# Kernel optimization log

Measured on AMD Instinct MI355X. Metric: run time of the kernel, lower is better.

Reference implementation:

```python
import jax, jax.numpy as jnp
import numpy as np

B, T, C, H = 4, 2048, 768, 12
D = C // H  # head_dim = 64
ROPE_BASE = 10000.0


def _make_rope_cache(seq_len, n_elem, base=ROPE_BASE):
    theta = 1.0 / base ** (jnp.arange(0, n_elem, 2, dtype=jnp.float32) / n_elem)  # [D/2]
    idx_theta = jnp.arange(seq_len, dtype=jnp.float32)[:, None] * theta[None, :]  # [T, D/2]
    return jnp.stack([jnp.cos(idx_theta), jnp.sin(idx_theta)], axis=-1)  # [T, D/2, 2]


def setup_inputs() -> dict:
    key = jax.random.key(0)
    k1, k2, k3 = jax.random.split(key, 3)
    x = jax.random.normal(k1, (B, T, C), dtype=jnp.float32)
    rope_cache = _make_rope_cache(T, D)
    w_qkv = jax.random.normal(k2, (3 * C, C), dtype=jnp.float32) * (1.0 / np.sqrt(C))
    w_o = jax.random.normal(k3, (C, C), dtype=jnp.float32) * (1.0 / np.sqrt(C))
    return {"x": x, "rope_cache": rope_cache, "w_qkv": w_qkv, "w_o": w_o}


def _apply_rope(t, cos, sin):
    # t: [B,T,H,D]; cos/sin: [T,D/2] broadcast to [1,T,1,D/2]
    tp = t.reshape(t.shape[:-1] + (D // 2, 2))
    t0, t1 = tp[..., 0], tp[..., 1]
    c = cos[None, :, None, :]
    s = sin[None, :, None, :]
    rot = jnp.stack([t0 * c - t1 * s, t0 * s + t1 * c], axis=-1)
    return rot.reshape(t.shape)


def reference(x, rope_cache, w_qkv, w_o):
    b, t, c = x.shape
    qkv = (x @ w_qkv.T).reshape(b, t, 3, H, D)
    q, k, v = qkv[:, :, 0], qkv[:, :, 1], qkv[:, :, 2]  # [B,T,H,D]
    cos = rope_cache[:t, :, 0]
    sin = rope_cache[:t, :, 1]
    q = _apply_rope(q, cos, sin)
    k = _apply_rope(k, cos, sin)
    scale = 1.0 / np.sqrt(D)
    att = jnp.einsum('bqhd,bkhd->bhqk', q, k) * scale  # [B,H,T,T]
    causal = jnp.tril(jnp.ones((t, t), dtype=bool))
    att = jnp.where(causal[None, None], att, jnp.finfo(att.dtype).min)
    att = jax.nn.softmax(att, axis=-1)
    y = jnp.einsum('bhqk,bkhd->bqhd', att, v).reshape(b, t, c)
    return y @ w_o.T
```

## Files before the change

kernel.cpp:

```cpp
#include <hip/hip_runtime.h>

#define B_  4
#define T_  2048
#define C_  768
#define H_  12
#define D_  64

typedef unsigned short u16;
typedef unsigned int   u32;
typedef __bf16 bf16;
typedef __bf16 bf16x4 __attribute__((ext_vector_type(4)));
typedef __bf16 bf16x8 __attribute__((ext_vector_type(8)));
typedef float  f32x4  __attribute__((ext_vector_type(4)));
typedef float  f32x16 __attribute__((ext_vector_type(16)));
typedef u32    u32x4  __attribute__((ext_vector_type(4)));
typedef __attribute__((address_space(1))) void* gas_t;
typedef __attribute__((address_space(3))) void* las_t;

static __device__ __forceinline__ u16 f2bf(float f) {
  u32 u = __builtin_bit_cast(u32, f);
  u += 0x7FFFu + ((u >> 16) & 1u);
  return (u16)(u >> 16);
}

static __device__ __forceinline__ u32 cvtpk(float a, float b) {
  u32 r;
  asm("v_cvt_pk_bf16_f32 %0, %1, %2" : "=v"(r) : "v"(a), "v"(b));
  return r;
}
static __device__ __forceinline__ void plswap(u32& a, u32& b) {
  asm volatile("v_permlane32_swap_b32 %0, %1" : "+v"(a), "+v"(b));
}

__global__ __launch_bounds__(256) void k_cvt3(const float* __restrict__ a0,
                                              const float* __restrict__ a1,
                                              const float* __restrict__ a2,
                                              u16* __restrict__ o0,
                                              u16* __restrict__ o1,
                                              u16* __restrict__ o2) {
  const int bid = blockIdx.x;
  const int tid = threadIdx.x;
  if (bid < 6144) {
    const int i = bid * 256 + tid;
    const float4 v = ((const float4*)a0)[i];
    ushort4 o;
    o.x = f2bf(v.x); o.y = f2bf(v.y); o.z = f2bf(v.z); o.w = f2bf(v.w);
    ((ushort4*)o0)[i] = o;
  } else if (bid < 7872) {
    const int i = (bid - 6144) * 256 + tid;
    const int n = i / 192;
    const int c4 = i - n * 192;
    int n2 = n;
    if (n < 1536) {
      const int d = n & 63;
      const int c = (((d & 1) | ((d >> 5) << 1)) << 4) | ((d >> 1) & 15);
      n2 = (n & ~63) | c;
    }
    const float4 v = ((const float4*)a1)[i];
    ushort4 o;
    o.x = f2bf(v.x); o.y = f2bf(v.y); o.z = f2bf(v.z); o.w = f2bf(v.w);
    ((ushort4*)o1)[n2 * 192 + c4] = o;
  } else {
    const int i = (bid - 7872) * 256 + tid;
    const float4 v = ((const float4*)a2)[i];
    ushort4 o;
    o.x = f2bf(v.x); o.y = f2bf(v.y); o.z = f2bf(v.z); o.w = f2bf(v.w);
    ((ushort4*)o2)[i] = o;
  }
}

template<int MODE, int BM>
__global__ __launch_bounds__(256) void k_gemm_bt(const u16* __restrict__ A,
                                                 const u16* __restrict__ Bt,
                                                 float* __restrict__ Cout,
                                                 u16* __restrict__ qout,
                                                 u16* __restrict__ kout,
                                                 u16* __restrict__ vout,
                                                 const float* __restrict__ rope,
                                                 int M, int N, int K) {
  constexpr int NJ = (BM == 128) ? 4 : 2;
  constexpr int PA = BM / 32;
  constexpr int NB = (BM == 64) ? 2 : 1;
  __shared__ u16 lA[NB * BM * 64];
  __shared__ u16 lB[NB * 128 * 64];
  const int tid = threadIdx.x;
  const int l = tid & 63, w = tid >> 6;
  const int lo = l & 15, hi = l >> 4;
  const int wrow = (BM == 128) ? (w >> 1) * 64 : 0;
  const int wcol = (BM == 128) ? (w & 1) * 64 : w * 32;
  const int pid = blockIdx.x + gridDim.x * blockIdx.y;
  const int total = gridDim.x * gridDim.y;
  const int lid = (pid & 7) * (total >> 3) + (pid >> 3);
  const int bx = lid % gridDim.x, by = lid / gridDim.x;
  const int m0 = by * BM, n0 = bx * 128;

  const int srow_t = tid >> 3;
  const int scb   = ((tid & 7) * 16) ^ ((srow_t & 7) << 4);
  const int swz   = (lo & 7) << 4;

  auto STAGE = [&](int bufi, int k0) {
#pragma unroll
    for (int p = 0; p < PA; ++p)
      __builtin_amdgcn_global_load_lds(
          (gas_t)(u16*)(A + (size_t)(m0 + srow_t + 32 * p) * K + k0 + (scb >> 1)),
          (las_t)(lA + bufi * BM * 64 + p * 2048 + tid * 8), 16, 0, 0);
#pragma unroll
    for (int p = 0; p < 4; ++p)
      __builtin_amdgcn_global_load_lds(
          (gas_t)(u16*)(Bt + (size_t)(n0 + srow_t + 32 * p) * K + k0 + (scb >> 1)),
          (las_t)(lB + bufi * 128 * 64 + p * 2048 + tid * 8), 16, 0, 0);
  };

  f32x4 acc[4][NJ] = {};
  auto COMPUTE = [&](const u16* la, const u16* lb) {
#pragma unroll
    for (int kk = 0; kk < 2; ++kk) {
      const int co = ((kk * 64 + hi * 16) ^ swz) >> 1;
      bf16x8 af[4], bfr[NJ];
#pragma unroll
      for (int i = 0; i < 4; ++i)
        af[i] = *(const bf16x8*)(la + (wrow + i * 16 + lo) * 64 + co);
#pragma unroll
      for (int j = 0; j < NJ; ++j)
        bfr[j] = *(const bf16x8*)(lb + (wcol + j * 16 + lo) * 64 + co);
      __builtin_amdgcn_s_setprio(1);
#pragma unroll
      for (int i = 0; i < 4; ++i)
#pragma unroll
        for (int j = 0; j < NJ; ++j)
          acc[i][j] = __builtin_amdgcn_mfma_f32_16x16x32_bf16(af[i], bfr[j], acc[i][j], 0, 0, 0);
      __builtin_amdgcn_s_setprio(0);
    }
  };

  if (BM == 128) {
    for (int k0 = 0; k0 < K; k0 += 64) {
      STAGE(0, k0);
      asm volatile("s_waitcnt vmcnt(0)" ::: "memory");
      __builtin_amdgcn_s_barrier();
      __builtin_amdgcn_sched_barrier(0);
      COMPUTE(lA, lB);
      asm volatile("" ::: "memory");
      __builtin_amdgcn_s_barrier();
      __builtin_amdgcn_sched_barrier(0);
    }
  } else {
    STAGE(0, 0);
    asm volatile("s_waitcnt vmcnt(0)" ::: "memory");
    __builtin_amdgcn_s_barrier();
    __builtin_amdgcn_sched_barrier(0);
    int cur = 0;
    const int nk = K >> 6;
    for (int ks = 0; ks < nk; ++ks) {
      if (ks + 1 < nk) {
        STAGE(cur ^ 1, (ks + 1) * 64);
        asm volatile("s_waitcnt vmcnt(6)" ::: "memory");
      } else {
        asm volatile("s_waitcnt vmcnt(0)" ::: "memory");
      }
      __builtin_amdgcn_s_barrier();
      __builtin_amdgcn_sched_barrier(0);
      COMPUTE(lA + cur * BM * 64, lB + cur * 128 * 64);
      asm volatile("" ::: "memory");
      __builtin_amdgcn_s_barrier();
      __builtin_amdgcn_sched_barrier(0);
      cur ^= 1;
    }
  }

  const int crow = m0 + wrow;
  if (MODE == 1) {
#pragma unroll
    for (int i = 0; i < 4; ++i)
#pragma unroll
      for (int j = 0; j < NJ; ++j)
#pragma unroll
        for (int r = 0; r < 4; ++r)
          Cout[(size_t)(crow + i * 16 + hi * 4 + r) * N + n0 + wcol + j * 16 + lo] = acc[i][j][r];
  } else {
    const int wc = w & 1;
    const int sect = bx / 6;
    const int h2 = (bx % 6) * 2 + wc;
    if (sect < 2) {
      const float qsc = (sect == 0) ? 0.18033688011f : 1.0f;
      u16* dst = (sect == 0) ? qout : kout;
#pragma unroll
      for (int i = 0; i < 4; ++i)
#pragma unroll
        for (int r = 0; r < 4; ++r) {
          const int trow = crow + i * 16 + hi * 4 + r;
          const int t = trow & (T_ - 1), bb = trow >> 11;
          const float2 cs0 = *(const float2*)(rope + ((size_t)t * 32 + lo) * 2);
          const float2 cs1 = *(const float2*)(rope + ((size_t)t * 32 + 16 + lo) * 2);
          const float a0 = acc[i][0][r], a1 = acc[i][1][r];
          const float a2 = acc[i][2][r], a3 = acc[i][3][r];
          const float e0 = (a0 * cs0.x - a1 * cs0.y) * qsc;
          const float e1 = (a0 * cs0.y + a1 * cs0.x) * qsc;
          const float e2 = (a2 * cs1.x - a3 * cs1.y) * qsc;
          const float e3 = (a2 * cs1.y + a3 * cs1.x) * qsc;
          u16* row = dst + ((size_t)(bb * H_ + h2) * T_ + t) * D_;
          *(ushort2*)(row + 2 * lo)      = make_ushort2(f2bf(e0), f2bf(e1));
          *(ushort2*)(row + 32 + 2 * lo) = make_ushort2(f2bf(e2), f2bf(e3));
        }
    } else {
#pragma unroll
      for (int i = 0; i < 4; ++i)
#pragma unroll
        for (int j = 0; j < NJ; ++j)
#pragma unroll
          for (int r = 0; r < 4; ++r) {
            const int trow = crow + i * 16 + hi * 4 + r;
            vout[(size_t)trow * C_ + h2 * D_ + j * 16 + lo] = f2bf(acc[i][j][r]);
          }
    }
  }
}

__global__ __launch_bounds__(256) void k_vtrans(const u16* __restrict__ vtmp,
                                                u16* __restrict__ vt) {
  __shared__ u16 lds[64][68];
  const int bid = blockIdx.x;
  const int ttile = bid & 31, bh = bid >> 5;
  const int b = bh / H_, h = bh % H_;
  const int tid = threadIdx.x;
  const int tl = tid >> 2, doff = (tid & 3) * 16;
  const u16* src = vtmp + (size_t)(b * T_ + ttile * 64 + tl) * C_ + h * D_ + doff;
  const uint4 v0 = *(const uint4*)(src);
  const uint4 v1 = *(const uint4*)(src + 8);
  *(uint2*)&lds[tl][doff + 0]  = make_uint2(v0.x, v0.y);
  *(uint2*)&lds[tl][doff + 4]  = make_uint2(v0.z, v0.w);
  *(uint2*)&lds[tl][doff + 8]  = make_uint2(v1.x, v1.y);
  *(uint2*)&lds[tl][doff + 12] = make_uint2(v1.z, v1.w);
  __syncthreads();
  const int d = tl, toff = doff;
  uint4 o0, o1;
#define PK(j) ((u32)lds[toff + (j)][d] | ((u32)lds[toff + (j) + 1][d] << 16))
  o0.x = PK(0);  o0.y = PK(2);  o0.z = PK(4);  o0.w = PK(6);
  o1.x = PK(8);  o1.y = PK(10); o1.z = PK(12); o1.w = PK(14);
#undef PK
  u16* dst = vt + ((size_t)bh * D_ + d) * T_ + ttile * 64 + toff;
  *(uint4*)(dst) = o0;
  *(uint4*)(dst + 8) = o1;
}

__global__ __launch_bounds__(256) void k_attn(const u16* __restrict__ qb,
                                              const u16* __restrict__ kb,
                                              const u16* __restrict__ vtb,
                                              u16* __restrict__ yb) {
  __shared__ u16 kbuf[2][64 * 64];
  __shared__ u16 vbuf[2][64 * 64];
  const int tid = threadIdx.x;
  const int w = tid >> 6, l = tid & 63;
  const int q5 = l & 31, hf = l >> 5;
  const int pid = blockIdx.x;
  const int xcd = pid & 7;
  const int rank = pid >> 3;
  const int wv = rank >> 5, ps = rank & 31;
  const int widx = wv * 32 + ((wv & 1) ? 31 - ps : ps);
  const int bh_local = widx % 6;
  const int bx = 15 - widx / 6;
  const int bh = xcd * 6 + bh_local;
  const int h = bh % H_, b = bh / H_;
  const u16* Q  = qb  + (size_t)bh * T_ * D_;
  const u16* K  = kb  + (size_t)bh * T_ * D_;
  const u16* Vt = vtb + (size_t)bh * D_ * T_;
  const int nt = 2 * bx + 2;
  const int q0w = bx * 128 + w * 32;
  const int q = q0w + q5;

  const int srow = tid >> 3;
  const int scb  = ((tid & 7) * 16) ^ ((srow & 7) << 4);

#define STAGE(bufi, j0s)                                                             \
  do {                                                                               \
    __builtin_amdgcn_global_load_lds((gas_t)(u16*)(K + (size_t)((j0s) + srow) * D_ + (scb >> 1)),      \
                                     (las_t)(&kbuf[bufi][0] + tid * 8), 16, 0, 0);   \
    __builtin_amdgcn_global_load_lds((gas_t)(u16*)(K + (size_t)((j0s) + 32 + srow) * D_ + (scb >> 1)), \
                                     (las_t)(&kbuf[bufi][0] + (tid + 256) * 8), 16, 0, 0);             \
    __builtin_amdgcn_global_load_lds((gas_t)(u16*)(Vt + (size_t)srow * T_ + (j0s) + (scb >> 1)),       \
                                     (las_t)(&vbuf[bufi][0] + tid * 8), 16, 0, 0);   \
    __builtin_amdgcn_global_load_lds((gas_t)(u16*)(Vt + (size_t)(32 + srow) * T_ + (j0s) + (scb >> 1)),\
                                     (las_t)(&vbuf[bufi][0] + (tid + 256) * 8), 16, 0, 0);             \
  } while (0)

  bf16x8 qf[4];
#pragma unroll
  for (int dc = 0; dc < 4; ++dc)
    qf[dc] = *(const bf16x8*)(Q + (size_t)q * D_ + dc * 16 + hf * 8);

  const f32x16 Z = {};
  f32x16 o0 = {}, o1 = {};
  float ls0 = 0.f, ls1 = 0.f, ls2 = 0.f, ls3 = 0.f;

  STAGE(0, 0);
  asm volatile("s_waitcnt vmcnt(0)" ::: "memory");
  __builtin_amdgcn_s_barrier();
  __builtin_amdgcn_sched_barrier(0);
  int cur = 0;
  for (int t = 0; t < nt; ++t) {
    const int j0 = t * 64;
    if (t + 1 < nt) {
      STAGE(cur ^ 1, (t + 1) * 64);
      asm volatile("s_waitcnt vmcnt(4)" ::: "memory");
    } else {
      asm volatile("s_waitcnt vmcnt(0)" ::: "memory");
    }
    __builtin_amdgcn_s_barrier();
    __builtin_amdgcn_sched_barrier(0);
    if (j0 <= q0w + 31) {
      const u16* kb_l = &kbuf[cur][0];
      const u16* vb_l = &vbuf[cur][0];
      const int swz = (l & 7) << 4;
#pragma unroll
      for (int st = 0; st < 2; ++st) {
        f32x16 s;
        __builtin_amdgcn_s_setprio(1);
        {
          const int krow = st * 32 + q5;
          const bf16x8 kd0 = *(const bf16x8*)(kb_l + krow * 64 + (((0   + 16 * hf) ^ swz) >> 1));
          s = __builtin_amdgcn_mfma_f32_32x32x16_bf16(kd0, qf[0], Z, 0, 0, 0);
          const bf16x8 kd1 = *(const bf16x8*)(kb_l + krow * 64 + (((32  + 16 * hf) ^ swz) >> 1));
          s = __builtin_amdgcn_mfma_f32_32x32x16_bf16(kd1, qf[1], s, 0, 0, 0);
          const bf16x8 kd2 = *(const bf16x8*)(kb_l + krow * 64 + (((64  + 16 * hf) ^ swz) >> 1));
          s = __builtin_amdgcn_mfma_f32_32x32x16_bf16(kd2, qf[2], s, 0, 0, 0);
          const bf16x8 kd3 = *(const bf16x8*)(kb_l + krow * 64 + (((96  + 16 * hf) ^ swz) >> 1));
          s = __builtin_amdgcn_mfma_f32_32x32x16_bf16(kd3, qf[3], s, 0, 0, 0);
        }
        __builtin_amdgcn_s_setprio(0);
        if (j0 + 63 > q0w) {
#pragma unroll
          for (int r = 0; r < 16; ++r) {
            const int kv = j0 + 32 * st + (r & 3) + 8 * (r >> 2) + 4 * hf;
            if (kv > q) s[r] = -1e30f;
          }
        }
#pragma unroll
        for (int r = 0; r < 16; ++r)
          s[r] = __builtin_amdgcn_exp2f(s[r]);
#pragma unroll
        for (int r = 0; r < 16; r += 4) {
          ls0 += s[r];
          ls1 += s[r + 1];
          ls2 += s[r + 2];
          ls3 += s[r + 3];
        }
        u32 a0 = cvtpk(s[0],  s[1]),  b0 = cvtpk(s[4],  s[5]);  plswap(a0, b0);
        u32 a1 = cvtpk(s[2],  s[3]),  b1 = cvtpk(s[6],  s[7]);  plswap(a1, b1);
        u32 a2 = cvtpk(s[8],  s[9]),  b2 = cvtpk(s[12], s[13]); plswap(a2, b2);
        u32 a3 = cvtpk(s[10], s[11]), b3 = cvtpk(s[14], s[15]); plswap(a3, b3);
        const bf16x8 pa0 = __builtin_bit_cast(bf16x8, (u32x4){a0, a1, b0, b1});
        const bf16x8 pa1 = __builtin_bit_cast(bf16x8, (u32x4){a2, a3, b2, b3});
        __builtin_amdgcn_s_setprio(1);
        {
          const int ks0 = st * 2, ks1 = st * 2 + 1;
          const bf16x8 vf00 = *(const bf16x8*)(vb_l + q5 * 64        + (((ks0 * 32 + 16 * hf) ^ swz) >> 1));
          const bf16x8 vf10 = *(const bf16x8*)(vb_l + (32 + q5) * 64 + (((ks0 * 32 + 16 * hf) ^ swz) >> 1));
          o0 = __builtin_amdgcn_mfma_f32_32x32x16_bf16(vf00, pa0, o0, 0, 0, 0);
          o1 = __builtin_amdgcn_mfma_f32_32x32x16_bf16(vf10, pa0, o1, 0, 0, 0);
          const bf16x8 vf01 = *(const bf16x8*)(vb_l + q5 * 64        + (((ks1 * 32 + 16 * hf) ^ swz) >> 1));
          const bf16x8 vf11 = *(const bf16x8*)(vb_l + (32 + q5) * 64 + (((ks1 * 32 + 16 * hf) ^ swz) >> 1));
          o0 = __builtin_amdgcn_mfma_f32_32x32x16_bf16(vf01, pa1, o0, 0, 0, 0);
          o1 = __builtin_amdgcn_mfma_f32_32x32x16_bf16(vf11, pa1, o1, 0, 0, 0);
        }
        __builtin_amdgcn_s_setprio(0);
      }
    }
    asm volatile("" ::: "memory");
    __builtin_amdgcn_s_barrier();
    __builtin_amdgcn_sched_barrier(0);
    cur ^= 1;
  }
#undef STAGE
  const float lsum = (ls0 + ls1) + (ls2 + ls3);
  const float lt = lsum + __shfl_xor(lsum, 32);
  const float linv = 1.0f / lt;
  u16* yrow = yb + (size_t)(b * T_ + q) * C_ + h * D_;
#pragma unroll
  for (int g = 0; g < 4; ++g) {
    bf16x4 ok0, ok1;
#pragma unroll
    for (int r = 0; r < 4; ++r) {
      ok0[r] = (__bf16)(o0[4 * g + r] * linv);
      ok1[r] = (__bf16)(o1[4 * g + r] * linv);
    }
    *(bf16x4*)(yrow + g * 8 + 4 * hf)      = ok0;
    *(bf16x4*)(yrow + 32 + g * 8 + 4 * hf) = ok1;
  }
}

extern "C" void kernel_launch(void* const* d_in, const int* in_sizes, int n_in,
                              void* d_out, int out_size, void* d_ws, size_t ws_size,
                              hipStream_t stream) {
  (void)in_sizes; (void)n_in; (void)out_size; (void)ws_size;
  const float* x    = (const float*)d_in[0];
  const float* rope = (const float*)d_in[1];
  const float* wqkv = (const float*)d_in[2];
  const float* wo   = (const float*)d_in[3];
  float* out = (float*)d_out;
  char* ws = (char*)d_ws;
  u16* xb    = (u16*)(ws);
  u16* wqkvb = (u16*)(ws + 12582912);
  u16* wob   = (u16*)(ws + 16121856);
  u16* vtmp  = (u16*)(ws + 17301504);
  u16* qb    = (u16*)(ws + 55050240);
  u16* kb    = (u16*)(ws + 67633152);
  u16* vtb   = (u16*)(ws + 80216064);
  u16* yb    = xb;

  k_cvt3<<<8448, 256, 0, stream>>>(x, wqkv, wo, xb, wqkvb, wob);
  k_gemm_bt<2, 128><<<dim3(18, 64), 256, 0, stream>>>(xb, wqkvb, nullptr, qb, kb, vtmp,
                                                      rope, 8192, 2304, 768);
  k_vtrans<<<1536, 256, 0, stream>>>(vtmp, vtb);
  k_attn<<<768, 256, 0, stream>>>(qb, kb, vtb, yb);
  k_gemm_bt<1, 64><<<dim3(6, 128), 256, 0, stream>>>(yb, wob, out, nullptr, nullptr, nullptr,
                                                     nullptr, 8192, 768, 768);
}
```

Baseline: 127.4 us.

## Pair causal query segments per block and split KV halves across waves

Each attention block now handles two 64-row query segments, p and 31-p, so every block walks the same total of 33 KV tiles in one flat pipelined loop. Within a block, wave pairs split each 64-key tile into two 32-key halves rather than one wave covering the whole tile. The partial outputs and row sums are then combined through LDS before the normalized result is written. This is meant to remove load imbalance across causal blocks and the dependence on the old snake ordering of the block schedule. In exchange it adds an LDS reduction, extra barriers at segment boundaries, a Q reload mid-loop, and idle waves on diagonal tiles.

```diff
diff --git a/kernel.cpp b/kernel.cpp
--- a/kernel.cpp
+++ b/kernel.cpp
@@ -249,27 +249,27 @@
                                               u16* __restrict__ yb) {
   __shared__ u16 kbuf[2][64 * 64];
   __shared__ u16 vbuf[2][64 * 64];
+  __shared__ float obuf[2][64][33];
+  __shared__ float lbuf[2][64];
   const int tid = threadIdx.x;
   const int w = tid >> 6, l = tid & 63;
   const int q5 = l & 31, hf = l >> 5;
+  const int qg = w >> 1, st = w & 1;
   const int pid = blockIdx.x;
   const int xcd = pid & 7;
   const int rank = pid >> 3;
-  const int wv = rank >> 5, ps = rank & 31;
-  const int widx = wv * 32 + ((wv & 1) ? 31 - ps : ps);
-  const int bh_local = widx % 6;
-  const int bx = 15 - widx / 6;
-  const int bh = xcd * 6 + bh_local;
+  const int p = rank / 6;
+  const int bh = xcd * 6 + rank % 6;
   const int h = bh % H_, b = bh / H_;
   const u16* Q  = qb  + (size_t)bh * T_ * D_;
   const u16* K  = kb  + (size_t)bh * T_ * D_;
   const u16* Vt = vtb + (size_t)bh * D_ * T_;
-  const int nt = 2 * bx + 2;
-  const int q0w = bx * 128 + w * 32;
-  const int q = q0w + q5;
+  const int segA = 16 + p, segB = 15 - p;
+  const int ntA = segA + 1;
 
   const int srow = tid >> 3;
   const int scb  = ((tid & 7) * 16) ^ ((srow & 7) << 4);
+  const int swz  = (l & 7) << 4;
 
 #define STAGE(bufi, j0s)                                                             \
   do {                                                                               \
@@ -283,6 +283,9 @@
                                      (las_t)(&vbuf[bufi][0] + (tid + 256) * 8), 16, 0, 0);             \
   } while (0)
 
+  int seg = segA;
+  int q0w = seg * 64 + qg * 32;
+  int q = q0w + q5;
   bf16x8 qf[4];
 #pragma unroll
   for (int dc = 0; dc < 4; ++dc)
@@ -297,95 +300,117 @@
   __builtin_amdgcn_s_barrier();
   __builtin_amdgcn_sched_barrier(0);
   int cur = 0;
-  for (int t = 0; t < nt; ++t) {
-    const int j0 = t * 64;
-    if (t + 1 < nt) {
-      STAGE(cur ^ 1, (t + 1) * 64);
+  for (int flat = 0; flat < 33; ++flat) {
+    const int local = (flat < ntA) ? flat : flat - ntA;
+    const int j0 = local * 64;
+    if (flat + 1 < 33) {
+      const int nloc = (flat + 1 < ntA) ? flat + 1 : flat + 1 - ntA;
+      STAGE(cur ^ 1, nloc * 64);
       asm volatile("s_waitcnt vmcnt(4)" ::: "memory");
     } else {
       asm volatile("s_waitcnt vmcnt(0)" ::: "memory");
     }
     __builtin_amdgcn_s_barrier();
     __builtin_amdgcn_sched_barrier(0);
-    if (j0 <= q0w + 31) {
+    if (j0 + 32 * st <= q0w + 31) {
       const u16* kb_l = &kbuf[cur][0];
       const u16* vb_l = &vbuf[cur][0];
-      const int swz = (l & 7) << 4;
-#pragma unroll
-      for (int st = 0; st < 2; ++st) {
-        f32x16 s;
-        __builtin_amdgcn_s_setprio(1);
-        {
-          const int krow = st * 32 + q5;
-          const bf16x8 kd0 = *(const bf16x8*)(kb_l + krow * 64 + (((0   + 16 * hf) ^ swz) >> 1));
-          s = __builtin_amdgcn_mfma_f32_32x32x16_bf16(kd0, qf[0], Z, 0, 0, 0);
-          const bf16x8 kd1 = *(const bf16x8*)(kb_l + krow * 64 + (((32  + 16 * hf) ^ swz) >> 1));
-          s = __builtin_amdgcn_mfma_f32_32x32x16_bf16(kd1, qf[1], s, 0, 0, 0);
-          const bf16x8 kd2 = *(const bf16x8*)(kb_l + krow * 64 + (((64  + 16 * hf) ^ swz) >> 1));
-          s = __builtin_amdgcn_mfma_f32_32x32x16_bf16(kd2, qf[2], s, 0, 0, 0);
-          const bf16x8 kd3 = *(const bf16x8*)(kb_l + krow * 64 + (((96  + 16 * hf) ^ swz) >> 1));
-          s = __builtin_amdgcn_mfma_f32_32x32x16_bf16(kd3, qf[3], s, 0, 0, 0);
+      f32x16 s;
+      __builtin_amdgcn_s_setprio(1);
+      {
+        const int krow = st * 32 + q5;
+        const bf16x8 kd0 = *(const bf16x8*)(kb_l + krow * 64 + (((0  + 16 * hf) ^ swz) >> 1));
+        s = __builtin_amdgcn_mfma_f32_32x32x16_bf16(kd0, qf[0], Z, 0, 0, 0);
+        const bf16x8 kd1 = *(const bf16x8*)(kb_l + krow * 64 + (((32 + 16 * hf) ^ swz) >> 1));
+        s = __builtin_amdgcn_mfma_f32_32x32x16_bf16(kd1, qf[1], s, 0, 0, 0);
+        const bf16x8 kd2 = *(const bf16x8*)(kb_l + krow * 64 + (((64 + 16 * hf) ^ swz) >> 1));
+        s = __builtin_amdgcn_mfma_f32_32x32x16_bf16(kd2, qf[2], s, 0, 0, 0);
+        const bf16x8 kd3 = *(const bf16x8*)(kb_l + krow * 64 + (((96 + 16 * hf) ^ swz) >> 1));
+        s = __builtin_amdgcn_mfma_f32_32x32x16_bf16(kd3, qf[3], s, 0, 0, 0);
+      }
+      __builtin_amdgcn_s_setprio(0);
+      if (local == seg) {
+#pragma unroll
+        for (int r = 0; r < 16; ++r) {
+          const int kv = j0 + 32 * st + (r & 3) + 8 * (r >> 2) + 4 * hf;
+          if (kv > q) s[r] = -1e30f;
         }
-        __builtin_amdgcn_s_setprio(0);
-        if (j0 + 63 > q0w) {
-#pragma unroll
-          for (int r = 0; r < 16; ++r) {
-            const int kv = j0 + 32 * st + (r & 3) + 8 * (r >> 2) + 4 * hf;
-            if (kv > q) s[r] = -1e30f;
-          }
-        }
-#pragma unroll
-        for (int r = 0; r < 16; ++r)
-          s[r] = __builtin_amdgcn_exp2f(s[r]);
-#pragma unroll
-        for (int r = 0; r < 16; r += 4) {
-          ls0 += s[r];
-          ls1 += s[r + 1];
-          ls2 += s[r + 2];
-          ls3 += s[r + 3];
-        }
-        u32 a0 = cvtpk(s[0],  s[1]),  b0 = cvtpk(s[4],  s[5]);  plswap(a0, b0);
-        u32 a1 = cvtpk(s[2],  s[3]),  b1 = cvtpk(s[6],  s[7]);  plswap(a1, b1);
-        u32 a2 = cvtpk(s[8],  s[9]),  b2 = cvtpk(s[12], s[13]); plswap(a2, b2);
-        u32 a3 = cvtpk(s[10], s[11]), b3 = cvtpk(s[14], s[15]); plswap(a3, b3);
-        const bf16x8 pa0 = __builtin_bit_cast(bf16x8, (u32x4){a0, a1, b0, b1});
-        const bf16x8 pa1 = __builtin_bit_cast(bf16x8, (u32x4){a2, a3, b2, b3});
-        __builtin_amdgcn_s_setprio(1);
-        {
-          const int ks0 = st * 2, ks1 = st * 2 + 1;
-          const bf16x8 vf00 = *(const bf16x8*)(vb_l + q5 * 64        + (((ks0 * 32 + 16 * hf) ^ swz) >> 1));
-          const bf16x8 vf10 = *(const bf16x8*)(vb_l + (32 + q5) * 64 + (((ks0 * 32 + 16 * hf) ^ swz) >> 1));
-          o0 = __builtin_amdgcn_mfma_f32_32x32x16_bf16(vf00, pa0, o0, 0, 0, 0);
-          o1 = __builtin_amdgcn_mfma_f32_32x32x16_bf16(vf10, pa0, o1, 0, 0, 0);
-          const bf16x8 vf01 = *(const bf16x8*)(vb_l + q5 * 64        + (((ks1 * 32 + 16 * hf) ^ swz) >> 1));
-          const bf16x8 vf11 = *(const bf16x8*)(vb_l + (32 + q5) * 64 + (((ks1 * 32 + 16 * hf) ^ swz) >> 1));
-          o0 = __builtin_amdgcn_mfma_f32_32x32x16_bf16(vf01, pa1, o0, 0, 0, 0);
-          o1 = __builtin_amdgcn_mfma_f32_32x32x16_bf16(vf11, pa1, o1, 0, 0, 0);
-        }
-        __builtin_amdgcn_s_setprio(0);
-      }
+      }
+#pragma unroll
+      for (int r = 0; r < 16; ++r)
+        s[r] = __builtin_amdgcn_exp2f(s[r]);
+#pragma unroll
+      for (int r = 0; r < 16; r += 4) {
+        ls0 += s[r]; ls1 += s[r + 1]; ls2 += s[r + 2]; ls3 += s[r + 3];
+      }
+      u32 a0 = cvtpk(s[0],  s[1]),  b0 = cvtpk(s[4],  s[5]);  plswap(a0, b0);
+      u32 a1 = cvtpk(s[2],  s[3]),  b1 = cvtpk(s[6],  s[7]);  plswap(a1, b1);
+      u32 a2 = cvtpk(s[8],  s[9]),  b2 = cvtpk(s[12], s[13]); plswap(a2, b2);
+      u32 a3 = cvtpk(s[10], s[11]), b3 = cvtpk(s[14], s[15]); plswap(a3, b3);
+      const bf16x8 pa0 = __builtin_bit_cast(bf16x8, (u32x4){a0, a1, b0, b1});
+      const bf16x8 pa1 = __builtin_bit_cast(bf16x8, (u32x4){a2, a3, b2, b3});
+      __builtin_amdgcn_s_setprio(1);
+      {
+        const int ks0 = st * 2, ks1 = st * 2 + 1;
+        const bf16x8 vf00 = *(const bf16x8*)(vb_l + q5 * 64        + (((ks0 * 32 + 16 * hf) ^ swz) >> 1));
+        const bf16x8 vf10 = *(const bf16x8*)(vb_l + (32 + q5) * 64 + (((ks0 * 32 + 16 * hf) ^ swz) >> 1));
+        o0 = __builtin_amdgcn_mfma_f32_32x32x16_bf16(vf00, pa0, o0, 0, 0, 0);
+        o1 = __builtin_amdgcn_mfma_f32_32x32x16_bf16(vf10, pa0, o1, 0, 0, 0);
+        const bf16x8 vf01 = *(const bf16x8*)(vb_l + q5 * 64        + (((ks1 * 32 + 16 * hf) ^ swz) >> 1));
+        const bf16x8 vf11 = *(const bf16x8*)(vb_l + (32 + q5) * 64 + (((ks1 * 32 + 16 * hf) ^ swz) >> 1));
+        o0 = __builtin_amdgcn_mfma_f32_32x32x16_bf16(vf01, pa1, o0, 0, 0, 0);
+        o1 = __builtin_amdgcn_mfma_f32_32x32x16_bf16(vf11, pa1, o1, 0, 0, 0);
+      }
+      __builtin_amdgcn_s_setprio(0);
+    }
+    if (local == seg && st == 1) {
+      float* ob = &obuf[qg][l][0];
+#pragma unroll
+      for (int r = 0; r < 16; ++r) { ob[r] = o0[r]; ob[16 + r] = o1[r]; }
+      float lr = (ls0 + ls1) + (ls2 + ls3);
+      lr += __shfl_xor(lr, 32);
+      lbuf[qg][l] = lr;
+      asm volatile("s_waitcnt lgkmcnt(0)" ::: "memory");
     }
     asm volatile("" ::: "memory");
     __builtin_amdgcn_s_barrier();
     __builtin_amdgcn_sched_barrier(0);
+    if (local == seg) {
+      if (st == 0) {
+        const float* ob = &obuf[qg][l][0];
+#pragma unroll
+        for (int r = 0; r < 16; ++r) { o0[r] += ob[r]; o1[r] += ob[16 + r]; }
+        float lr = (ls0 + ls1) + (ls2 + ls3);
+        lr += __shfl_xor(lr, 32);
+        const float lt = lr + lbuf[qg][l];
+        const float linv = 1.0f / lt;
+        u16* yrow = yb + (size_t)(b * T_ + q) * C_ + h * D_;
+#pragma unroll
+        for (int g = 0; g < 4; ++g) {
+          bf16x4 ok0, ok1;
+#pragma unroll
+          for (int r = 0; r < 4; ++r) {
+            ok0[r] = (__bf16)(o0[4 * g + r] * linv);
+            ok1[r] = (__bf16)(o1[4 * g + r] * linv);
+          }
+          *(bf16x4*)(yrow + g * 8 + 4 * hf)      = ok0;
+          *(bf16x4*)(yrow + 32 + g * 8 + 4 * hf) = ok1;
+        }
+      }
+      if (flat < 32) {
+        seg = segB;
+        q0w = seg * 64 + qg * 32;
+        q = q0w + q5;
+#pragma unroll
+        for (int dc = 0; dc < 4; ++dc)
+          qf[dc] = *(const bf16x8*)(Q + (size_t)q * D_ + dc * 16 + hf * 8);
+      }
+      o0 = Z; o1 = Z;
+      ls0 = 0.f; ls1 = 0.f; ls2 = 0.f; ls3 = 0.f;
+    }
     cur ^= 1;
   }
 #undef STAGE
-  const float lsum = (ls0 + ls1) + (ls2 + ls3);
-  const float lt = lsum + __shfl_xor(lsum, 32);
-  const float linv = 1.0f / lt;
-  u16* yrow = yb + (size_t)(b * T_ + q) * C_ + h * D_;
-#pragma unroll
-  for (int g = 0; g < 4; ++g) {
-    bf16x4 ok0, ok1;
-#pragma unroll
-    for (int r = 0; r < 4; ++r) {
-      ok0[r] = (__bf16)(o0[4 * g + r] * linv);
-      ok1[r] = (__bf16)(o1[4 * g + r] * linv);
-    }
-    *(bf16x4*)(yrow + g * 8 + 4 * hf)      = ok0;
-    *(bf16x4*)(yrow + 32 + g * 8 + 4 * hf) = ok1;
-  }
 }
 
 extern "C" void kernel_launch(void* const* d_in, const int* in_sizes, int n_in,
```

Result: faster. 122.8 us (-3.6%).
